# Performance work log

Hardware: AMD Instinct MI355X
Metric: run time of the kernel (lower is better)

The kernel has to match this reference:

```python
import jax, jax.numpy as jnp
import numpy as np

N = 1681  # 41*41, fixed by the /1681 normalization in the original loss
BS = 32

def setup_inputs() -> dict:
    key = jax.random.key(0)
    k1, k2 = jax.random.split(key)
    pred = jax.random.normal(k1, (BS, N, N), dtype=jnp.float32)
    target = jax.random.normal(k2, (BS, N, N), dtype=jnp.float32)
    return {"pred": pred, "target": target}

def _col_scale_by_row_norm(x):
    # no = 1/sqrt(sum_k x[l, j, k]^2)  -> per-row L2 norm reciprocal, shape [bs, N]
    # x @ diag(no) scales COLUMN j by no[j]; replace O(N^2 D) matmul with
    inv_rn = 1.0 / jnp.sqrt(jnp.sum(x * x, axis=2))  # [bs, N]
    return x * inv_rn[:, None, :]

def reference(pred, target):
    bs = pred.shape[0]
    p = _col_scale_by_row_norm(pred)
    t = _col_scale_by_row_norm(target)
    losses = -jnp.sum(p * t, axis=(1, 2))  # [bs]
    return jnp.sum(losses) / bs / 1681.0
```

## Files before the change

### kernel.cpp

```cpp
#include <hip/hip_runtime.h>

#define N 1681
#define BS 32
#define BAND 41
#define NBLOCKS (BS * BAND)
#define THREADS 256
#define NROWS_TOTAL (BS * N)


__global__ __launch_bounds__(THREADS) void zero_kernel(float* __restrict__ dcol) {
  const int idx = blockIdx.x * THREADS + threadIdx.x;
  if (idx < NROWS_TOTAL) dcol[idx] = 0.0f;
}

__global__ __launch_bounds__(THREADS) void pass1_kernel(
    const float* __restrict__ pred,
    const float* __restrict__ targ,
    float* __restrict__ sp,
    float* __restrict__ st,
    float* __restrict__ dcol) {
  __shared__ float dsum[N];

  const int b    = blockIdx.x;
  const int tid  = threadIdx.x;
  const int lane = tid & 63;
  const int wid  = tid >> 6;
  const int l    = b / BAND;
  const long R0  = (long)b * BAND;

  for (int idx = tid; idx < N; idx += THREADS) dsum[idx] = 0.0f;
  __syncthreads();

  const float4* __restrict__ pred4 = (const float4*)pred;
  const float4* __restrict__ targ4 = (const float4*)targ;

  const int h = wid;
  float dprod[7][4];
#pragma unroll
  for (int t2 = 0; t2 < 7; ++t2)
#pragma unroll
    for (int ee = 0; ee < 4; ++ee) dprod[t2][ee] = 0.0f;

  const int rr0 = (wid - (int)(R0 & 3)) & 3;

  for (int rr = rr0; rr < BAND; rr += 4) {
    const long R = R0 + rr;
    const long s = R * (long)N;
    const long q = s >> 2;

    float psq = 0.0f, tsq = 0.0f;
#pragma unroll
    for (int t2 = 0; t2 < 7; ++t2) {
      const long c = q + t2 * 64 + lane;
      if (t2 < 6 || lane < 37) {
        const float4 p4 = pred4[c];
        const float4 t4 = targ4[c];
        const float pv[4] = {p4.x, p4.y, p4.z, p4.w};
        const float tv[4] = {t4.x, t4.y, t4.z, t4.w};
        if (t2 == 0 || t2 == 6) {
          const int colb = t2 * 256 + 4 * lane - h;
#pragma unroll
          for (int ee = 0; ee < 4; ++ee) {
            const bool ok = (unsigned)(colb + ee) < (unsigned)N;
            const float pm = ok ? pv[ee] : 0.0f;
            const float tm = ok ? tv[ee] : 0.0f;
            psq = fmaf(pm, pm, psq);
            tsq = fmaf(tm, tm, tsq);
            dprod[t2][ee] = fmaf(pm, tm, dprod[t2][ee]);
          }
        } else {
#pragma unroll
          for (int ee = 0; ee < 4; ++ee) {
            psq = fmaf(pv[ee], pv[ee], psq);
            tsq = fmaf(tv[ee], tv[ee], tsq);
            dprod[t2][ee] = fmaf(pv[ee], tv[ee], dprod[t2][ee]);
          }
        }
      }
    }

#pragma unroll
    for (int off = 32; off > 0; off >>= 1) {
      psq += __shfl_down(psq, off, 64);
      tsq += __shfl_down(tsq, off, 64);
    }
    if (lane == 0) {
      sp[R] = psq;
      st[R] = tsq;
    }
  }

#pragma unroll
  for (int t2 = 0; t2 < 7; ++t2)
#pragma unroll
    for (int ee = 0; ee < 4; ++ee) {
      const int col = t2 * 256 + 4 * lane + ee - h;
      if ((unsigned)col < (unsigned)N) atomicAdd(&dsum[col], dprod[t2][ee]);
    }
  __syncthreads();

  for (int idx = tid; idx < N; idx += THREADS)
    atomicAdd(&dcol[(size_t)l * N + idx], dsum[idx]);
}

__global__ __launch_bounds__(THREADS) void fin1_kernel(
    const float* __restrict__ sp,
    const float* __restrict__ st,
    const float* __restrict__ dcol,
    float* __restrict__ bsums) {
  __shared__ double red[4];

  double acc = 0.0;
  for (int g = blockIdx.x * THREADS + threadIdx.x; g < NROWS_TOTAL;
       g += gridDim.x * THREADS) {
    const double s = (double)sp[g] * (double)st[g];
    acc += (double)dcol[g] / sqrt(s);
  }
#pragma unroll
  for (int off = 32; off > 0; off >>= 1) acc += __shfl_down(acc, off, 64);
  const int wid = threadIdx.x >> 6;
  if ((threadIdx.x & 63) == 0) red[wid] = acc;
  __syncthreads();
  if (threadIdx.x == 0)
    bsums[blockIdx.x] = (float)(red[0] + red[1] + red[2] + red[3]);
}

__global__ __launch_bounds__(64) void fin2_kernel(
    const float* __restrict__ bsums, float* __restrict__ out) {
  double acc = (double)bsums[threadIdx.x];
#pragma unroll
  for (int off = 32; off > 0; off >>= 1) acc += __shfl_down(acc, off, 64);
  if (threadIdx.x == 0)
    out[0] = (float)(-acc / ((double)BS * (double)N));
}

extern "C" void kernel_launch(void* const* d_in, const int* in_sizes, int n_in,
                              void* d_out, int out_size, void* d_ws, size_t ws_size,
                              hipStream_t stream) {
  const float* pred = (const float*)d_in[0];
  const float* targ = (const float*)d_in[1];

  float* ws    = (float*)d_ws;
  float* sp    = ws;
  float* st    = ws + (size_t)NROWS_TOTAL;
  float* dcol  = ws + (size_t)2 * NROWS_TOTAL;
  float* bsums = ws + (size_t)3 * NROWS_TOTAL;

  zero_kernel<<<(NROWS_TOTAL + THREADS - 1) / THREADS, THREADS, 0, stream>>>(dcol);
  pass1_kernel<<<NBLOCKS, THREADS, 0, stream>>>(pred, targ, sp, st, dcol);
  fin1_kernel<<<64, THREADS, 0, stream>>>(sp, st, dcol, bsums);
  fin2_kernel<<<1, 64, 0, stream>>>(bsums, (float*)d_out);
}
```

Baseline: 172.1 us.

## Split row bands across two blocks, drop zero kernel, reduce partial column sums in finalize

Each 41-row band is now split across two blocks, doubling the grid and adding an occupancy hint to the launch bounds. Each block writes its column partial sums to a per-block buffer instead of doing global atomics, which removes the separate zeroing kernel. The finalize kernel sums 82 partials per column, and the inner loop software-prefetches the next float4 with clamped indices. This adds about 18 MB of partial-sum traffic and a strided gather in finalize in exchange for fewer atomics and more parallelism in the main pass.

```diff
diff --git a/kernel.cpp b/kernel.cpp
--- a/kernel.cpp
+++ b/kernel.cpp
@@ -2,31 +2,31 @@
 
 #define N 1681
 #define BS 32
-#define BAND 41
-#define NBLOCKS (BS * BAND)
 #define THREADS 256
 #define NROWS_TOTAL (BS * N)
+#define MAXC ((BS * N * N) / 4)
+#define NBLK (BS * 41 * 2)
+#define PARTS_PER_MAT 82
 
 
-__global__ __launch_bounds__(THREADS) void zero_kernel(float* __restrict__ dcol) {
-  const int idx = blockIdx.x * THREADS + threadIdx.x;
-  if (idx < NROWS_TOTAL) dcol[idx] = 0.0f;
-}
-
-__global__ __launch_bounds__(THREADS) void pass1_kernel(
+__global__ __launch_bounds__(THREADS, 8) void pass1_kernel(
     const float* __restrict__ pred,
     const float* __restrict__ targ,
     float* __restrict__ sp,
     float* __restrict__ st,
-    float* __restrict__ dcol) {
+    float* __restrict__ dpart) {
   __shared__ float dsum[N];
 
   const int b    = blockIdx.x;
   const int tid  = threadIdx.x;
   const int lane = tid & 63;
   const int wid  = tid >> 6;
-  const int l    = b / BAND;
-  const long R0  = (long)b * BAND;
+  const int band = b >> 1;
+  const int halfsel = b & 1;
+  const int Rbase = band * 41 + halfsel * 21;
+  const int nr    = halfsel ? 20 : 21;
+  const int h     = wid;
+  const int rr0   = (h - (Rbase & 3)) & 3;
 
   for (int idx = tid; idx < N; idx += THREADS) dsum[idx] = 0.0f;
   __syncthreads();
@@ -34,49 +34,49 @@
   const float4* __restrict__ pred4 = (const float4*)pred;
   const float4* __restrict__ targ4 = (const float4*)targ;
 
-  const int h = wid;
   float dprod[7][4];
 #pragma unroll
   for (int t2 = 0; t2 < 7; ++t2)
 #pragma unroll
     for (int ee = 0; ee < 4; ++ee) dprod[t2][ee] = 0.0f;
 
-  const int rr0 = (wid - (int)(R0 & 3)) & 3;
+  for (int rr = rr0; rr < nr; rr += 4) {
+    const int R = Rbase + rr;
+    const int q = (int)(((long)R * N) >> 2);
+    float psq = 0.0f, tsq = 0.0f;
 
-  for (int rr = rr0; rr < BAND; rr += 4) {
-    const long R = R0 + rr;
-    const long s = R * (long)N;
-    const long q = s >> 2;
-
-    float psq = 0.0f, tsq = 0.0f;
+    float4 pc = pred4[min(q + lane, MAXC - 1)];
+    float4 tc = targ4[min(q + lane, MAXC - 1)];
 #pragma unroll
     for (int t2 = 0; t2 < 7; ++t2) {
-      const long c = q + t2 * 64 + lane;
-      if (t2 < 6 || lane < 37) {
-        const float4 p4 = pred4[c];
-        const float4 t4 = targ4[c];
-        const float pv[4] = {p4.x, p4.y, p4.z, p4.w};
-        const float tv[4] = {t4.x, t4.y, t4.z, t4.w};
-        if (t2 == 0 || t2 == 6) {
-          const int colb = t2 * 256 + 4 * lane - h;
+      float4 pn, tn;
+      if (t2 < 6) {
+        const int c_ = min(q + (t2 + 1) * 64 + lane, MAXC - 1);
+        pn = pred4[c_];
+        tn = targ4[c_];
+      }
+      const float pv[4] = {pc.x, pc.y, pc.z, pc.w};
+      const float tv[4] = {tc.x, tc.y, tc.z, tc.w};
+      if (t2 == 0 || t2 == 6) {
+        const int colb = t2 * 256 + 4 * lane - h;
 #pragma unroll
-          for (int ee = 0; ee < 4; ++ee) {
-            const bool ok = (unsigned)(colb + ee) < (unsigned)N;
-            const float pm = ok ? pv[ee] : 0.0f;
-            const float tm = ok ? tv[ee] : 0.0f;
-            psq = fmaf(pm, pm, psq);
-            tsq = fmaf(tm, tm, tsq);
-            dprod[t2][ee] = fmaf(pm, tm, dprod[t2][ee]);
-          }
-        } else {
+        for (int ee = 0; ee < 4; ++ee) {
+          const bool ok = (unsigned)(colb + ee) < (unsigned)N;
+          const float pm = ok ? pv[ee] : 0.0f;
+          const float tm = ok ? tv[ee] : 0.0f;
+          psq = fmaf(pm, pm, psq);
+          tsq = fmaf(tm, tm, tsq);
+          dprod[t2][ee] = fmaf(pm, tm, dprod[t2][ee]);
+        }
+      } else {
 #pragma unroll
-          for (int ee = 0; ee < 4; ++ee) {
-            psq = fmaf(pv[ee], pv[ee], psq);
-            tsq = fmaf(tv[ee], tv[ee], tsq);
-            dprod[t2][ee] = fmaf(pv[ee], tv[ee], dprod[t2][ee]);
-          }
+        for (int ee = 0; ee < 4; ++ee) {
+          psq = fmaf(pv[ee], pv[ee], psq);
+          tsq = fmaf(tv[ee], tv[ee], tsq);
+          dprod[t2][ee] = fmaf(pv[ee], tv[ee], dprod[t2][ee]);
         }
       }
+      if (t2 < 6) { pc = pn; tc = tn; }
     }
 
 #pragma unroll
@@ -84,10 +84,7 @@
       psq += __shfl_down(psq, off, 64);
       tsq += __shfl_down(tsq, off, 64);
     }
-    if (lane == 0) {
-      sp[R] = psq;
-      st[R] = tsq;
-    }
+    if (lane == 0) { sp[R] = psq; st[R] = tsq; }
   }
 
 #pragma unroll
@@ -98,23 +95,27 @@
       if ((unsigned)col < (unsigned)N) atomicAdd(&dsum[col], dprod[t2][ee]);
     }
   __syncthreads();
-
   for (int idx = tid; idx < N; idx += THREADS)
-    atomicAdd(&dcol[(size_t)l * N + idx], dsum[idx]);
+    dpart[(size_t)b * N + idx] = dsum[idx];
 }
 
 __global__ __launch_bounds__(THREADS) void fin1_kernel(
     const float* __restrict__ sp,
     const float* __restrict__ st,
-    const float* __restrict__ dcol,
-    float* __restrict__ bsums) {
+    const float* __restrict__ dpart,
+    double* __restrict__ bsums) {
   __shared__ double red[4];
 
   double acc = 0.0;
   for (int g = blockIdx.x * THREADS + threadIdx.x; g < NROWS_TOTAL;
        g += gridDim.x * THREADS) {
+    const int l = g / N;
+    const int j = g - l * N;
+    const float* __restrict__ dp = dpart + (size_t)l * PARTS_PER_MAT * N + j;
+    float dv = 0.0f;
+    for (int p = 0; p < PARTS_PER_MAT; ++p) dv += dp[(size_t)p * N];
     const double s = (double)sp[g] * (double)st[g];
-    acc += (double)dcol[g] / sqrt(s);
+    acc += (double)dv / sqrt(s);
   }
 #pragma unroll
   for (int off = 32; off > 0; off >>= 1) acc += __shfl_down(acc, off, 64);
@@ -122,12 +123,12 @@
   if ((threadIdx.x & 63) == 0) red[wid] = acc;
   __syncthreads();
   if (threadIdx.x == 0)
-    bsums[blockIdx.x] = (float)(red[0] + red[1] + red[2] + red[3]);
+    bsums[blockIdx.x] = red[0] + red[1] + red[2] + red[3];
 }
 
 __global__ __launch_bounds__(64) void fin2_kernel(
-    const float* __restrict__ bsums, float* __restrict__ out) {
-  double acc = (double)bsums[threadIdx.x];
+    const double* __restrict__ bsums, float* __restrict__ out) {
+  double acc = bsums[threadIdx.x] + bsums[threadIdx.x + 64];
 #pragma unroll
   for (int off = 32; off > 0; off >>= 1) acc += __shfl_down(acc, off, 64);
   if (threadIdx.x == 0)
@@ -140,14 +141,12 @@
   const float* pred = (const float*)d_in[0];
   const float* targ = (const float*)d_in[1];
 
-  float* ws    = (float*)d_ws;
-  float* sp    = ws;
-  float* st    = ws + (size_t)NROWS_TOTAL;
-  float* dcol  = ws + (size_t)2 * NROWS_TOTAL;
-  float* bsums = ws + (size_t)3 * NROWS_TOTAL;
+  double* bsums = (double*)d_ws;
+  float*  dpart = (float*)(bsums + 128);
+  float*  sp    = dpart + (size_t)NBLK * N;
+  float*  st    = sp + (size_t)NROWS_TOTAL;
 
-  zero_kernel<<<(NROWS_TOTAL + THREADS - 1) / THREADS, THREADS, 0, stream>>>(dcol);
-  pass1_kernel<<<NBLOCKS, THREADS, 0, stream>>>(pred, targ, sp, st, dcol);
-  fin1_kernel<<<64, THREADS, 0, stream>>>(sp, st, dcol, bsums);
+  pass1_kernel<<<NBLK, THREADS, 0, stream>>>(pred, targ, sp, st, dpart);
+  fin1_kernel<<<128, THREADS, 0, stream>>>(sp, st, dpart, bsums);
   fin2_kernel<<<1, 64, 0, stream>>>(bsums, (float*)d_out);
 }
```

Result: slower. 324.1 us (+88.3%).
